# Performance work log

Measured on AMD Instinct MI355X. Metric: run time of the kernel, lower is better.

The kernel has to match this reference:

```python
import jax, jax.numpy as jnp
import numpy as np

V, E, H, L, B, S = 50000, 512, 512, 2, 4, 256
DIN = 2 * E  # == 2*H, layer input size for all layers
GH = 4 * H   # torch LSTM gate order: i, f, g, o


def _lstm_dir(x, mask, w_ih, w_hh, b, reverse):
    """One direction of one LSTM layer with packed-sequence semantics.
    x: [B,S,DIN], mask: [B,S] bool. Returns [B,S,H]; padded steps emit 0
    and do not update state (matches pack_padded/pad_packed behavior)."""
    xs = jnp.swapaxes(x, 0, 1)                      # [S,B,DIN]
    ms = jnp.swapaxes(mask, 0, 1)[..., None]        # [S,B,1]
    pre = jnp.einsum('sbd,gd->sbg', xs, w_ih) + b   # input projection, [S,B,4H]

    def step(carry, inp):
        h, c = carry
        px, m = inp
        g = px + h @ w_hh.T
        i, f, gg, o = jnp.split(g, 4, axis=-1)
        c_new = jax.nn.sigmoid(f) * c + jax.nn.sigmoid(i) * jnp.tanh(gg)
        h_new = jax.nn.sigmoid(o) * jnp.tanh(c_new)
        h = jnp.where(m, h_new, h)
        c = jnp.where(m, c_new, c)
        return (h, c), jnp.where(m, h_new, jnp.zeros_like(h_new))

    init = (jnp.zeros((x.shape[0], H), x.dtype), jnp.zeros((x.shape[0], H), x.dtype))
    _, outs = jax.lax.scan(step, init, (pre, ms), reverse=reverse)
    return jnp.swapaxes(outs, 0, 1)                 # [B,S,H]


def setup_inputs() -> dict:
    key = jax.random.key(0)
    ks = jax.random.split(key, 12)
    sentence = jax.random.randint(ks[0], (B, S), 0, V)
    pos = jax.random.randint(ks[1], (B, S), 0, V)
    length = jax.random.randint(ks[2], (B,), S // 2, S + 1)
    length = length.at[0].set(S)  # ensure max(length) == S for static shapes
    emb = jax.random.normal(ks[3], (V, E), jnp.float32) * 0.02
    emb = emb.at[0].set(0.0)      # padding_idx row is zero
    sc = 1.0 / np.sqrt(H)
    w_ih = jax.random.uniform(ks[4], (L, 2, GH, DIN), jnp.float32, -sc, sc)
    w_hh = jax.random.uniform(ks[5], (L, 2, GH, H), jnp.float32, -sc, sc)
    b_ih = jax.random.uniform(ks[6], (L, 2, GH), jnp.float32, -sc, sc)
    b_hh = jax.random.uniform(ks[7], (L, 2, GH), jnp.float32, -sc, sc)
    s1 = 1.0 / np.sqrt(4 * H)
    w1 = jax.random.uniform(ks[8], (H, 4 * H), jnp.float32, -s1, s1)
    b1 = jax.random.uniform(ks[9], (H,), jnp.float32, -s1, s1)
    s2 = 1.0 / np.sqrt(H)
    w2 = jax.random.uniform(ks[10], (1, H), jnp.float32, -s2, s2)
    b2 = jax.random.uniform(ks[11], (1,), jnp.float32, -s2, s2)
    return {"sentence": sentence, "pos": pos, "length": length, "emb": emb,
            "w_ih": w_ih, "w_hh": w_hh, "b_ih": b_ih, "b_hh": b_hh,
            "w1": w1, "b1": b1, "w2": w2, "b2": b2}


def reference(sentence, pos, length, emb, w_ih, w_hh, b_ih, b_hh, w1, b1, w2, b2):
    x = jnp.concatenate([emb[sentence], emb[pos]], axis=-1)   # [B,S,2E]
    mask = jnp.arange(S)[None, :] < length[:, None]           # [B,S]
    for l in range(L):
        fwd = _lstm_dir(x, mask, w_ih[l, 0], w_hh[l, 0], b_ih[l, 0] + b_hh[l, 0], False)
        bwd = _lstm_dir(x, mask, w_ih[l, 1], w_hh[l, 1], b_ih[l, 1] + b_hh[l, 1], True)
        x = jnp.concatenate([fwd, bwd], axis=-1)              # [B,S,2H]
    # pairwise concat [feat_i ; feat_j] @ w1 == split w1 and broadcast-add
    wa, wb = w1[:, :2 * H], w1[:, 2 * H:]
    pa = jnp.einsum('bsd,hd->bsh', x, wa)                     # [B,S,H]
    pb = jnp.einsum('btd,hd->bth', x, wb)                     # [B,S,H]
    hmid = jnp.tanh(pa[:, :, None, :] + pb[:, None, :, :] + b1)  # [B,S,S,H]
    score = jnp.einsum('bsth,h->bst', hmid, w2[0]) + b2[0]    # [B,S,S]
    return score
```

## Files before the change

### kernel.cpp

```cpp
#include <hip/hip_runtime.h>

typedef unsigned int u32;
typedef unsigned short u16;
typedef unsigned long long u64;
typedef short bf16x8 __attribute__((ext_vector_type(8)));
typedef float f32x4 __attribute__((ext_vector_type(4)));

#define B_   4
#define S_   256
#define H_   512
#define GH_  2048
#define DIN_ 1024
#define M_   1024
#define WG_PER_DIR 64

__device__ __forceinline__ float bf2f(u16 u){
  union { u32 i; float f; } v; v.i = ((u32)u) << 16; return v.f;
}
__device__ __forceinline__ u16 f2bf(float f){
  union { float f; u32 i; } v; v.f = f;
  u32 r = v.i + 0x7fffu + ((v.i >> 16) & 1u);
  return (u16)(r >> 16);
}
__device__ __forceinline__ float sigm(float x){ return 1.f/(1.f + __expf(-x)); }
__device__ __forceinline__ float tanhfast(float x){
  float e = __expf(2.f*x); return 1.f - 2.f/(e + 1.f);
}
__device__ __forceinline__ void split8(const float* __restrict__ p,
                                       bf16x8& h, bf16x8& l){
  #pragma unroll
  for (int j = 0; j < 8; ++j){
    float f = p[j];
    u16 hh = f2bf(f);
    h[j] = (short)hh;
    l[j] = (short)f2bf(f - bf2f(hh));
  }
}

__global__ __launch_bounds__(256) void split_w(
    const float* __restrict__ src, u16* __restrict__ hi, u16* __restrict__ lo,
    int n4)
{
  int i = blockIdx.x*256 + threadIdx.x;
  if (i >= n4) return;
  float4 f = ((const float4*)src)[i];
  u16 h0 = f2bf(f.x), h1 = f2bf(f.y), h2 = f2bf(f.z), h3 = f2bf(f.w);
  u16 l0 = f2bf(f.x - bf2f(h0)), l1 = f2bf(f.y - bf2f(h1));
  u16 l2 = f2bf(f.z - bf2f(h2)), l3 = f2bf(f.w - bf2f(h3));
  ((u64*)hi)[i] = (u64)h0 | ((u64)h1<<16) | ((u64)h2<<32) | ((u64)h3<<48);
  ((u64*)lo)[i] = (u64)l0 | ((u64)l1<<16) | ((u64)l2<<32) | ((u64)l3<<48);
}

__global__ __launch_bounds__(256) void embed_kernel(
    const int* __restrict__ sent, const int* __restrict__ pos,
    const float* __restrict__ emb,
    u16* __restrict__ xhi, u16* __restrict__ xlo)
{
  const int m = blockIdx.x, tid = threadIdx.x;
  const int si = sent[m], pi = pos[m];
  const float2* es = (const float2*)(emb + (size_t)si * H_);
  const float2* ep = (const float2*)(emb + (size_t)pi * H_);
  float2 a = es[tid];
  float2 b = ep[tid];
  u32* xh = (u32*)(xhi + (size_t)m * DIN_);
  u32* xl = (u32*)(xlo + (size_t)m * DIN_);
  u16 ax = f2bf(a.x), ay = f2bf(a.y);
  u16 bx = f2bf(b.x), by = f2bf(b.y);
  xh[tid]       = (u32)ax | ((u32)ay << 16);
  xh[256 + tid] = (u32)bx | ((u32)by << 16);
  u16 axl = f2bf(a.x - bf2f(ax)), ayl = f2bf(a.y - bf2f(ay));
  u16 bxl = f2bf(b.x - bf2f(bx)), byl = f2bf(b.y - bf2f(by));
  xl[tid]       = (u32)axl | ((u32)ayl << 16);
  xl[256 + tid] = (u32)bxl | ((u32)byl << 16);
}

__global__ __launch_bounds__(256,2) void gemm_bf16(
    const u16* __restrict__ Ah, const u16* __restrict__ Al,
    const u16* __restrict__ Bh, const u16* __restrict__ Bl, int ldb, int perm,
    const float* __restrict__ bias1, const float* __restrict__ bias2,
    float* __restrict__ C, int N, int K)
{
  const int lane = threadIdx.x & 63, wave = threadIdx.x >> 6;
  const int m0 = blockIdx.y*64 + (wave>>1)*32;
  const int n0 = blockIdx.x*64 + (wave&1)*32;
  const int r15 = lane & 15, quad = lane >> 4;
  const u16* a0 = Ah + (size_t)(m0 + r15)*K + quad*8;
  const u16* a1 = a0 + (size_t)16*K;
  const u16* l0 = Al + (size_t)(m0 + r15)*K + quad*8;
  const u16* l1 = l0 + (size_t)16*K;
  const int nA = n0 + r15, nB = nA + 16;
  const int rA = perm ? ((nA&3)*H_ + (nA>>2)) : nA;
  const int rB = perm ? ((nB&3)*H_ + (nB>>2)) : nB;
  const u16* bh0 = Bh + (size_t)rA*ldb + quad*8;
  const u16* bh1 = Bh + (size_t)rB*ldb + quad*8;
  const u16* bl0 = Bl + (size_t)rA*ldb + quad*8;
  const u16* bl1 = Bl + (size_t)rB*ldb + quad*8;
  f32x4 acc00 = {0.f,0.f,0.f,0.f}, acc01 = acc00, acc10 = acc00, acc11 = acc00;
  for (int k = 0; k < K; k += 32){
    bf16x8 va0 = *(const bf16x8*)(a0 + k);
    bf16x8 va1 = *(const bf16x8*)(a1 + k);
    bf16x8 vl0 = *(const bf16x8*)(l0 + k);
    bf16x8 vl1 = *(const bf16x8*)(l1 + k);
    bf16x8 wh0 = *(const bf16x8*)(bh0 + k);
    bf16x8 wh1 = *(const bf16x8*)(bh1 + k);
    bf16x8 wl0v = *(const bf16x8*)(bl0 + k);
    bf16x8 wl1v = *(const bf16x8*)(bl1 + k);
    acc00 = __builtin_amdgcn_mfma_f32_16x16x32_bf16(va0, wh0, acc00, 0,0,0);
    acc00 = __builtin_amdgcn_mfma_f32_16x16x32_bf16(vl0, wh0, acc00, 0,0,0);
    acc00 = __builtin_amdgcn_mfma_f32_16x16x32_bf16(va0, wl0v, acc00, 0,0,0);
    acc01 = __builtin_amdgcn_mfma_f32_16x16x32_bf16(va0, wh1, acc01, 0,0,0);
    acc01 = __builtin_amdgcn_mfma_f32_16x16x32_bf16(vl0, wh1, acc01, 0,0,0);
    acc01 = __builtin_amdgcn_mfma_f32_16x16x32_bf16(va0, wl1v, acc01, 0,0,0);
    acc10 = __builtin_amdgcn_mfma_f32_16x16x32_bf16(va1, wh0, acc10, 0,0,0);
    acc10 = __builtin_amdgcn_mfma_f32_16x16x32_bf16(vl1, wh0, acc10, 0,0,0);
    acc10 = __builtin_amdgcn_mfma_f32_16x16x32_bf16(va1, wl0v, acc10, 0,0,0);
    acc11 = __builtin_amdgcn_mfma_f32_16x16x32_bf16(va1, wh1, acc11, 0,0,0);
    acc11 = __builtin_amdgcn_mfma_f32_16x16x32_bf16(vl1, wh1, acc11, 0,0,0);
    acc11 = __builtin_amdgcn_mfma_f32_16x16x32_bf16(va1, wl1v, acc11, 0,0,0);
  }
  float bA = 0.f, bB = 0.f;
  if (bias1){ bA += bias1[rA]; bB += bias1[rB]; }
  if (bias2){ bA += bias2[rA]; bB += bias2[rB]; }
  const int mr = m0 + quad*4;
  #pragma unroll
  for (int r = 0; r < 4; ++r){
    C[(size_t)(mr + r)*N + nA]      = acc00[r] + bA;
    C[(size_t)(mr + r)*N + nB]      = acc01[r] + bB;
    C[(size_t)(mr + r + 16)*N + nA] = acc10[r] + bA;
    C[(size_t)(mr + r + 16)*N + nB] = acc11[r] + bB;
  }
}

__global__ __launch_bounds__(256,2) void gemm_wT_x(
    const u16* __restrict__ Wh, const u16* __restrict__ Wl, int ldw,
    const u16* __restrict__ xh, const u16* __restrict__ xl,
    const float* __restrict__ biasM,
    float* __restrict__ CT, int K)
{
  const int lane = threadIdx.x & 63, wave = threadIdx.x >> 6;
  const int m0 = blockIdx.y*64 + (wave>>1)*32;
  const int n0 = blockIdx.x*64 + (wave&1)*32;
  const int b  = blockIdx.z;
  const int r15 = lane & 15, quad = lane >> 4;
  const u16* ah0 = Wh + (size_t)(m0 + r15)*ldw + quad*8;
  const u16* ah1 = ah0 + (size_t)16*ldw;
  const u16* al0 = Wl + (size_t)(m0 + r15)*ldw + quad*8;
  const u16* al1 = al0 + (size_t)16*ldw;
  const u16* bh0 = xh + (size_t)(b*S_ + n0 + r15)*DIN_ + quad*8;
  const u16* bh1 = bh0 + (size_t)16*DIN_;
  const u16* bl0 = xl + (size_t)(b*S_ + n0 + r15)*DIN_ + quad*8;
  const u16* bl1 = bl0 + (size_t)16*DIN_;
  f32x4 acc00 = {0.f,0.f,0.f,0.f}, acc01 = acc00, acc10 = acc00, acc11 = acc00;
  for (int k = 0; k < K; k += 32){
    bf16x8 vah0 = *(const bf16x8*)(ah0 + k);
    bf16x8 vah1 = *(const bf16x8*)(ah1 + k);
    bf16x8 val0 = *(const bf16x8*)(al0 + k);
    bf16x8 val1 = *(const bf16x8*)(al1 + k);
    bf16x8 vh0 = *(const bf16x8*)(bh0 + k);
    bf16x8 vh1 = *(const bf16x8*)(bh1 + k);
    bf16x8 vl0 = *(const bf16x8*)(bl0 + k);
    bf16x8 vl1 = *(const bf16x8*)(bl1 + k);
    acc00 = __builtin_amdgcn_mfma_f32_16x16x32_bf16(vah0, vh0, acc00, 0,0,0);
    acc00 = __builtin_amdgcn_mfma_f32_16x16x32_bf16(val0, vh0, acc00, 0,0,0);
    acc00 = __builtin_amdgcn_mfma_f32_16x16x32_bf16(vah0, vl0, acc00, 0,0,0);
    acc01 = __builtin_amdgcn_mfma_f32_16x16x32_bf16(vah0, vh1, acc01, 0,0,0);
    acc01 = __builtin_amdgcn_mfma_f32_16x16x32_bf16(val0, vh1, acc01, 0,0,0);
    acc01 = __builtin_amdgcn_mfma_f32_16x16x32_bf16(vah0, vl1, acc01, 0,0,0);
    acc10 = __builtin_amdgcn_mfma_f32_16x16x32_bf16(vah1, vh0, acc10, 0,0,0);
    acc10 = __builtin_amdgcn_mfma_f32_16x16x32_bf16(val1, vh0, acc10, 0,0,0);
    acc10 = __builtin_amdgcn_mfma_f32_16x16x32_bf16(vah1, vl0, acc10, 0,0,0);
    acc11 = __builtin_amdgcn_mfma_f32_16x16x32_bf16(vah1, vh1, acc11, 0,0,0);
    acc11 = __builtin_amdgcn_mfma_f32_16x16x32_bf16(val1, vh1, acc11, 0,0,0);
    acc11 = __builtin_amdgcn_mfma_f32_16x16x32_bf16(vah1, vl1, acc11, 0,0,0);
  }
  const int mr = m0 + quad*4;
  const int nA = n0 + r15, nB = nA + 16;
  #pragma unroll
  for (int r = 0; r < 4; ++r){
    float bia0 = biasM[mr + r];
    float bia1 = biasM[mr + r + 16];
    CT[(size_t)(b*H_ + mr + r)*S_ + nA]      = acc00[r] + bia0;
    CT[(size_t)(b*H_ + mr + r)*S_ + nB]      = acc01[r] + bia0;
    CT[(size_t)(b*H_ + mr + r + 16)*S_ + nA] = acc10[r] + bia1;
    CT[(size_t)(b*H_ + mr + r + 16)*S_ + nB] = acc11[r] + bia1;
  }
}

__global__ __launch_bounds__(128,1) void lstm_scan(
    const float* __restrict__ pre,
    const float* __restrict__ whh,
    const int* __restrict__ length,
    u32* __restrict__ Au32,
    u32* __restrict__ ctr,
    u32* __restrict__ xh32, u32* __restrict__ xl32)
{
  const int wg = blockIdx.x;
  const int dir = wg >> 6, lwg = wg & 63;
  const int tid = threadIdx.x, lane = tid & 63, wave = tid >> 6;
  const int r15 = lane & 15, quad = lane >> 4;
  const int tile = lwg*2 + wave;
  const int gpbase = tile*16;

  const float* wdir = whh + (size_t)dir*GH_*H_;
  const int gp = gpbase + r15;
  const int srow = (gp & 3)*H_ + (gp >> 2);
  bf16x8 wh[16], wl[16];
  #pragma unroll
  for (int kk = 0; kk < 16; ++kk)
    split8(wdir + (size_t)srow*H_ + kk*32 + quad*8, wh[kk], wl[kk]);

  const float* preD = pre + (size_t)dir*M_*GH_;
  const int myb = lane & 3;
  const int njg = tile*4 + ((lane >> 2) & 3);
  const int lenb = length[myb];
  const int base = lane & ~3;
  const int row = r15 & 7;
  u32* AbufD = Au32 + dir*4096;
  float h_state = 0.f, c_state = 0.f;

  for (int ss = 0; ss < S_; ++ss){
    const int s = dir ? (S_ - 1 - ss) : ss;
    const int rp = ss & 1;
    const u64* Ar64 = (const u64*)(AbufD + rp*2048);
    union { u64 d[2]; bf16x8 v; } ua[16];
    #pragma unroll
    for (int kk = 0; kk < 16; ++kk){
      ua[kk].d[0] = __hip_atomic_load(Ar64 + (size_t)row*128 + kk*8 + quad*2,
                                      __ATOMIC_RELAXED, __HIP_MEMORY_SCOPE_AGENT);
      ua[kk].d[1] = __hip_atomic_load(Ar64 + (size_t)row*128 + kk*8 + quad*2 + 1,
                                      __ATOMIC_RELAXED, __HIP_MEMORY_SCOPE_AGENT);
    }
    f32x4 acc = {0.f,0.f,0.f,0.f};
    #pragma unroll
    for (int kk = 0; kk < 16; ++kk){
      acc = __builtin_amdgcn_mfma_f32_16x16x32_bf16(ua[kk].v, wh[kk], acc, 0,0,0);
      acc = __builtin_amdgcn_mfma_f32_16x16x32_bf16(ua[kk].v, wl[kk], acc, 0,0,0);
    }
    float si = 0.f, sf = 0.f, sg = 0.f, so = 0.f;
    #pragma unroll
    for (int r = 0; r < 4; ++r){
      float gsum = acc[r] + __shfl(acc[r], lane ^ 16);
      float gpre = gsum + preD[(size_t)(r*S_ + s)*GH_ + gpbase + r15];
      float xi = __shfl(gpre, base + 0);
      float xf = __shfl(gpre, base + 1);
      float xg = __shfl(gpre, base + 2);
      float xo = __shfl(gpre, base + 3);
      if (r == myb){ si = xi; sf = xf; sg = xg; so = xo; }
    }
    float ctn = sigm(sf)*c_state + sigm(si)*tanhfast(sg);
    float htn = sigm(so)*tanhfast(ctn);
    const bool mk = (s < lenb);
    if (mk){ c_state = ctn; h_state = htn; }
    const float outv = mk ? htn : 0.f;
    u32 hv = f2bf(h_state);
    u32 hl = f2bf(h_state - bf2f((u16)hv));
    u32 ov = f2bf(outv);
    u32 ol = f2bf(outv - bf2f((u16)ov));
    u32 ph  = (u32)__shfl((int)hv, lane ^ 4);
    u32 pl  = (u32)__shfl((int)hl, lane ^ 4);
    u32 po  = (u32)__shfl((int)ov, lane ^ 4);
    u32 pol = (u32)__shfl((int)ol, lane ^ 4);
    if (lane < 16){
      u32* Aw = AbufD + (rp^1)*2048;
      const int p = njg >> 1;
      const int xw = (myb*S_ + s)*(DIN_/2) + dir*(H_/2) + p;
      if ((lane & 4) == 0){
        __hip_atomic_store(Aw + myb*256 + p, hv | (ph << 16),
                           __ATOMIC_RELAXED, __HIP_MEMORY_SCOPE_AGENT);
        xh32[xw] = ov | (po << 16);
      } else {
        __hip_atomic_store(Aw + (4+myb)*256 + p, pl | (hl << 16),
                           __ATOMIC_RELAXED, __HIP_MEMORY_SCOPE_AGENT);
        xl32[xw] = pol | (ol << 16);
      }
    }
    __syncthreads();
    if (tid == 0){
      __hip_atomic_fetch_add(&ctr[dir], 1u,
                             __ATOMIC_RELAXED, __HIP_MEMORY_SCOPE_AGENT);
      const u32 target = (u32)(ss + 1)*WG_PER_DIR;
      while (__hip_atomic_load(&ctr[dir], __ATOMIC_RELAXED,
                               __HIP_MEMORY_SCOPE_AGENT) < target){
        __builtin_amdgcn_s_sleep(1);
      }
    }
    __syncthreads();
  }
}

__global__ __launch_bounds__(256) void score_kernel(
    const float* __restrict__ pa, const float* __restrict__ pbT,
    const float* __restrict__ w2, const float* __restrict__ b2,
    float* __restrict__ out)
{
  const int bs = blockIdx.x;
  const int b = bs >> 8;
  const int t = threadIdx.x;
  __shared__ float pas[H_];
  __shared__ float w2s[H_];
  const float* paRow = pa + (size_t)bs*H_;
  for (int i = t; i < H_; i += 256){ pas[i] = paRow[i]; w2s[i] = w2[i]; }
  __syncthreads();
  const float* pbB = pbT + (size_t)b*H_*S_ + t;
  float acc = b2[0];
  #pragma unroll 4
  for (int h = 0; h < H_; ++h){
    float v = pas[h] + pbB[(size_t)h*S_];
    acc += w2s[h]*tanhfast(v);
  }
  out[(size_t)bs*S_ + t] = acc;
}

extern "C" void kernel_launch(void* const* d_in, const int* in_sizes, int n_in,
                              void* d_out, int out_size, void* d_ws, size_t ws_size,
                              hipStream_t stream)
{
  const int*   sent = (const int*)d_in[0];
  const int*   pos  = (const int*)d_in[1];
  const int*   len  = (const int*)d_in[2];
  const float* emb  = (const float*)d_in[3];
  const float* wih  = (const float*)d_in[4];
  const float* whh  = (const float*)d_in[5];
  const float* bih  = (const float*)d_in[6];
  const float* bhh  = (const float*)d_in[7];
  const float* w1   = (const float*)d_in[8];
  const float* b1   = (const float*)d_in[9];
  const float* w2   = (const float*)d_in[10];
  const float* b2   = (const float*)d_in[11];
  float* out = (float*)d_out;

  char* ws = (char*)d_ws;
  u32*   Au32  = (u32*)(ws);
  u32*   ctr   = (u32*)(ws + 32768);
  u16*   x0hi  = (u16*)(ws + ((size_t)1<<20));
  u16*   x0lo  = (u16*)(ws + ((size_t)3<<20));
  u16*   x1hi  = (u16*)(ws + ((size_t)5<<20));
  u16*   x1lo  = (u16*)(ws + ((size_t)7<<20));
  u16*   x2hi  = (u16*)(ws + ((size_t)9<<20));
  u16*   x2lo  = (u16*)(ws + ((size_t)11<<20));
  float* pa    = (float*)(ws + ((size_t)13<<20));
  float* pbT   = (float*)(ws + ((size_t)15<<20));
  float* pre   = (float*)(ws + ((size_t)17<<20));
  u16*   wihH  = (u16*)(ws + ((size_t)33<<20));
  u16*   wihL  = (u16*)(ws + ((size_t)49<<20));
  u16*   w1H   = (u16*)(ws + ((size_t)65<<20));
  u16*   w1L   = (u16*)(ws + ((size_t)67<<20));

  split_w<<<dim3(8192), dim3(256), 0, stream>>>(wih, wihH, wihL, 2097152);
  split_w<<<dim3(1024), dim3(256), 0, stream>>>(w1,  w1H,  w1L,   262144);

  embed_kernel<<<dim3(M_), dim3(256), 0, stream>>>(sent, pos, emb, x0hi, x0lo);

  for (int l = 0; l < 2; ++l){
    const u16* xh = l ? x1hi : x0hi;
    const u16* xl = l ? x1lo : x0lo;
    for (int d = 0; d < 2; ++d){
      const size_t wo = (size_t)(l*2+d)*GH_*DIN_;
      gemm_bf16<<<dim3(GH_/64, M_/64), dim3(256), 0, stream>>>(
        xh, xl, wihH + wo, wihL + wo, DIN_, 1,
        bih + (size_t)(l*2+d)*GH_, bhh + (size_t)(l*2+d)*GH_,
        pre + (size_t)d*M_*GH_, GH_, DIN_);
    }
    hipMemsetAsync(Au32, 0, 32768 + 64, stream);
    u16* oh = l ? x2hi : x1hi;
    u16* ol = l ? x2lo : x1lo;
    lstm_scan<<<dim3(2*WG_PER_DIR), dim3(128), 0, stream>>>(
        pre, whh + (size_t)l*2*GH_*H_, len, Au32, ctr, (u32*)oh, (u32*)ol);
  }

  gemm_bf16<<<dim3(H_/64, M_/64), dim3(256), 0, stream>>>(
      x2hi, x2lo, w1H, w1L, GH_, 0, nullptr, nullptr, pa, H_, DIN_);
  gemm_wT_x<<<dim3(S_/64, H_/64, B_), dim3(256), 0, stream>>>(
      w1H + DIN_, w1L + DIN_, GH_, x2hi, x2lo, b1, pbT, DIN_);
  score_kernel<<<dim3(M_), dim3(256), 0, stream>>>(pa, pbT, w2, b2, out);
}
```

Before: 3.118 ms.

## Halve scan workgroups, replace atomic counter barrier with per-WG flag polling, prefetch pre

Each direction's recurrent scan now runs on 32 workgroups of 4 waves instead of 64 workgroups of 2 waves, which cuts the number of participants in the cross-workgroup barrier. The shared atomic counter is replaced by per-workgroup step flags that one wave polls together with a wave-wide all-check. The barrier is skipped on the last step. The pre-activation value for the next step is prefetched during the current step, and the MFMA chain is split into four independent accumulators to shorten the dependency chain. The tradeoff is more waves per CU and one more vector add per step, and the flag protocol depends on relaxed atomics staying correctly ordered.

```diff
diff --git a/kernel.cpp b/kernel.cpp
--- a/kernel.cpp
+++ b/kernel.cpp
@@ -12,7 +12,7 @@
 #define GH_  2048
 #define DIN_ 1024
 #define M_   1024
-#define WG_PER_DIR 64
+#define WG_PER_DIR 32
 
 __device__ __forceinline__ float bf2f(u16 u){
   union { u32 i; float f; } v; v.i = ((u32)u) << 16; return v.f;
@@ -186,19 +186,19 @@
   }
 }
 
-__global__ __launch_bounds__(128,1) void lstm_scan(
+__global__ __launch_bounds__(256,1) void lstm_scan(
     const float* __restrict__ pre,
     const float* __restrict__ whh,
     const int* __restrict__ length,
     u32* __restrict__ Au32,
-    u32* __restrict__ ctr,
+    u32* __restrict__ flags,
     u32* __restrict__ xh32, u32* __restrict__ xl32)
 {
   const int wg = blockIdx.x;
-  const int dir = wg >> 6, lwg = wg & 63;
+  const int dir = wg >> 5, lwg = wg & 31;
   const int tid = threadIdx.x, lane = tid & 63, wave = tid >> 6;
   const int r15 = lane & 15, quad = lane >> 4;
-  const int tile = lwg*2 + wave;
+  const int tile = lwg*4 + wave;
   const int gpbase = tile*16;
 
   const float* wdir = whh + (size_t)dir*GH_*H_;
@@ -216,7 +216,16 @@
   const int base = lane & ~3;
   const int row = r15 & 7;
   u32* AbufD = Au32 + dir*4096;
+  u32* myflags = flags + dir*128;
   float h_state = 0.f, c_state = 0.f;
+
+  float pcur[4];
+  {
+    const int s0 = dir ? (S_-1) : 0;
+    #pragma unroll
+    for (int r = 0; r < 4; ++r)
+      pcur[r] = preD[(size_t)(r*S_ + s0)*GH_ + gpbase + r15];
+  }
 
   for (int ss = 0; ss < S_; ++ss){
     const int s = dir ? (S_ - 1 - ss) : ss;
@@ -230,17 +239,21 @@
       ua[kk].d[1] = __hip_atomic_load(Ar64 + (size_t)row*128 + kk*8 + quad*2 + 1,
                                       __ATOMIC_RELAXED, __HIP_MEMORY_SCOPE_AGENT);
     }
-    f32x4 acc = {0.f,0.f,0.f,0.f};
+    f32x4 a4[4];
+    #pragma unroll
+    for (int j = 0; j < 4; ++j) a4[j] = (f32x4){0.f,0.f,0.f,0.f};
     #pragma unroll
     for (int kk = 0; kk < 16; ++kk){
-      acc = __builtin_amdgcn_mfma_f32_16x16x32_bf16(ua[kk].v, wh[kk], acc, 0,0,0);
-      acc = __builtin_amdgcn_mfma_f32_16x16x32_bf16(ua[kk].v, wl[kk], acc, 0,0,0);
-    }
+      const int j = kk >> 2;
+      a4[j] = __builtin_amdgcn_mfma_f32_16x16x32_bf16(ua[kk].v, wh[kk], a4[j], 0,0,0);
+      a4[j] = __builtin_amdgcn_mfma_f32_16x16x32_bf16(ua[kk].v, wl[kk], a4[j], 0,0,0);
+    }
+    f32x4 acc = (a4[0] + a4[1]) + (a4[2] + a4[3]);
     float si = 0.f, sf = 0.f, sg = 0.f, so = 0.f;
     #pragma unroll
     for (int r = 0; r < 4; ++r){
       float gsum = acc[r] + __shfl(acc[r], lane ^ 16);
-      float gpre = gsum + preD[(size_t)(r*S_ + s)*GH_ + gpbase + r15];
+      float gpre = gsum + pcur[r];
       float xi = __shfl(gpre, base + 0);
       float xf = __shfl(gpre, base + 1);
       float xg = __shfl(gpre, base + 2);
@@ -252,6 +265,12 @@
     const bool mk = (s < lenb);
     if (mk){ c_state = ctn; h_state = htn; }
     const float outv = mk ? htn : 0.f;
+    if (ss + 1 < S_){
+      const int sn = dir ? (S_ - 2 - ss) : (ss + 1);
+      #pragma unroll
+      for (int r = 0; r < 4; ++r)
+        pcur[r] = preD[(size_t)(r*S_ + sn)*GH_ + gpbase + r15];
+    }
     u32 hv = f2bf(h_state);
     u32 hl = f2bf(h_state - bf2f((u16)hv));
     u32 ov = f2bf(outv);
@@ -260,7 +279,7 @@
     u32 pl  = (u32)__shfl((int)hl, lane ^ 4);
     u32 po  = (u32)__shfl((int)ov, lane ^ 4);
     u32 pol = (u32)__shfl((int)ol, lane ^ 4);
-    if (lane < 16){
+    if (wave == 0 && lane < 16){
       u32* Aw = AbufD + (rp^1)*2048;
       const int p = njg >> 1;
       const int xw = (myb*S_ + s)*(DIN_/2) + dir*(H_/2) + p;
@@ -273,18 +292,36 @@
                            __ATOMIC_RELAXED, __HIP_MEMORY_SCOPE_AGENT);
         xl32[xw] = pol | (ol << 16);
       }
-    }
-    __syncthreads();
-    if (tid == 0){
-      __hip_atomic_fetch_add(&ctr[dir], 1u,
-                             __ATOMIC_RELAXED, __HIP_MEMORY_SCOPE_AGENT);
-      const u32 target = (u32)(ss + 1)*WG_PER_DIR;
-      while (__hip_atomic_load(&ctr[dir], __ATOMIC_RELAXED,
-                               __HIP_MEMORY_SCOPE_AGENT) < target){
-        __builtin_amdgcn_s_sleep(1);
+    } else if (wave != 0 && lane < 16){
+      u32* Aw = AbufD + (rp^1)*2048;
+      const int p = njg >> 1;
+      const int xw = (myb*S_ + s)*(DIN_/2) + dir*(H_/2) + p;
+      if ((lane & 4) == 0){
+        __hip_atomic_store(Aw + myb*256 + p, hv | (ph << 16),
+                           __ATOMIC_RELAXED, __HIP_MEMORY_SCOPE_AGENT);
+        xh32[xw] = ov | (po << 16);
+      } else {
+        __hip_atomic_store(Aw + (4+myb)*256 + p, pl | (hl << 16),
+                           __ATOMIC_RELAXED, __HIP_MEMORY_SCOPE_AGENT);
+        xl32[xw] = pol | (ol << 16);
       }
     }
-    __syncthreads();
+    if (ss != S_ - 1){
+      __syncthreads();
+      if (tid == 0)
+        __hip_atomic_store(&myflags[lwg], (u32)(ss + 1),
+                           __ATOMIC_RELAXED, __HIP_MEMORY_SCOPE_AGENT);
+      if (wave == 0){
+        const u32 tgt = (u32)(ss + 1);
+        for (;;){
+          u32 f = __hip_atomic_load(&myflags[lane & 31],
+                                    __ATOMIC_RELAXED, __HIP_MEMORY_SCOPE_AGENT);
+          if (__all((int)(f >= tgt))) break;
+          __builtin_amdgcn_s_sleep(1);
+        }
+      }
+      __syncthreads();
+    }
   }
 }
 
@@ -331,7 +368,7 @@
 
   char* ws = (char*)d_ws;
   u32*   Au32  = (u32*)(ws);
-  u32*   ctr   = (u32*)(ws + 32768);
+  u32*   flags = (u32*)(ws + 32768);
   u16*   x0hi  = (u16*)(ws + ((size_t)1<<20));
   u16*   x0lo  = (u16*)(ws + ((size_t)3<<20));
   u16*   x1hi  = (u16*)(ws + ((size_t)5<<20));
@@ -361,11 +398,11 @@
         bih + (size_t)(l*2+d)*GH_, bhh + (size_t)(l*2+d)*GH_,
         pre + (size_t)d*M_*GH_, GH_, DIN_);
     }
-    hipMemsetAsync(Au32, 0, 32768 + 64, stream);
+    hipMemsetAsync(Au32, 0, 32768 + 1024, stream);
     u16* oh = l ? x2hi : x1hi;
     u16* ol = l ? x2lo : x1lo;
-    lstm_scan<<<dim3(2*WG_PER_DIR), dim3(128), 0, stream>>>(
-        pre, whh + (size_t)l*2*GH_*H_, len, Au32, ctr, (u32*)oh, (u32*)ol);
+    lstm_scan<<<dim3(2*WG_PER_DIR), dim3(256), 0, stream>>>(
+        pre, whh + (size_t)l*2*GH_*H_, len, Au32, flags, (u32*)oh, (u32*)ol);
   }
 
   gemm_bf16<<<dim3(H_/64, M_/64), dim3(256), 0, stream>>>(
```

Result: slower. 3.302 ms (+5.9%).
